# Kernel optimization log

Measured on AMD Instinct MI355X. Metric: run time of the kernel, lower is better.

## Reference

```python
import jax, jax.numpy as jnp
import numpy as np

N = 50000
E = 600000
D = 128


def gcn_conv(x, row, col, w, W, b):
    """PyG GCNConv: add self-loops (weight 1), symmetric deg^-1/2 normalization,
    linear transform, edge-weighted scatter-add aggregation, then bias."""
    n = x.shape[0]
    loop = jnp.arange(n)
    r = jnp.concatenate([row, loop])            # source nodes, [E+N]
    c = jnp.concatenate([col, loop])            # target nodes, [E+N]
    ww = jnp.concatenate([w, jnp.ones((n,), x.dtype)])
    deg = jax.ops.segment_sum(ww, c, num_segments=n)          # weighted in-degree
    dinv = jnp.where(deg > 0, jax.lax.rsqrt(deg), jnp.zeros_like(deg))
    norm = dinv[r] * ww * dinv[c]               # [E+N]
    xl = x @ W                                  # [n, D_out]
    msg = norm[:, None] * xl[r]                 # gather + scale, [E+N, D_out]
    out = jax.ops.segment_sum(msg, c, num_segments=n)
    return out + b


def setup_inputs() -> dict:
    key = jax.random.key(0)
    ks = jax.random.split(key, 12)
    x = jax.random.normal(ks[0], (N, D), dtype=jnp.float32)
    edge_index = jax.random.randint(ks[1], (2, E), 0, N, dtype=jnp.int64)
    edge_weights = jax.random.uniform(ks[2], (E,), dtype=jnp.float32)
    s = 1.0 / np.sqrt(D)
    W1 = jax.random.uniform(ks[3], (D, D), jnp.float32, -s, s)
    b1 = jnp.zeros((D,), jnp.float32)
    W2 = jax.random.uniform(ks[4], (D, D), jnp.float32, -s, s)
    b2 = jnp.zeros((D,), jnp.float32)
    W3 = jax.random.uniform(ks[5], (D, D), jnp.float32, -s, s)
    b3 = jnp.zeros((D,), jnp.float32)
    prelu_w = jnp.array(0.25, jnp.float32)
    return {"x": x, "edge_index": edge_index, "edge_weights": edge_weights,
            "W1": W1, "b1": b1, "W2": W2, "b2": b2, "W3": W3, "b3": b3,
            "prelu_w": prelu_w}


def reference(x, edge_index, edge_weights, W1, b1, W2, b2, W3, b3, prelu_w):
    row, col = edge_index[0], edge_index[1]
    # layer 1: GCNConv -> (dropout: eval, identity) -> ELU
    h = gcn_conv(x, row, col, edge_weights, W1, b1)
    h = jax.nn.elu(h)
    # layer 2: GCNConv -> GELU (torch default = exact erf)
    h = gcn_conv(h, row, col, edge_weights, W2, b2)
    h = jax.nn.gelu(h, approximate=False)
    # layer 3: GCNConv -> PReLU (learnable scalar slope)
    h = gcn_conv(h, row, col, edge_weights, W3, b3)
    h = jnp.where(h >= 0, h, prelu_w * h)
    return h
```

## Files before the change

### kernel.cpp

```cpp
#include <hip/hip_runtime.h>
#include <hip/hip_fp16.h>
#include <math.h>

constexpr int D = 128;

struct __align__(16) H8 { __half2 h[4]; };
struct __align__(8)  H4 { __half2 a, b; };


__device__ __forceinline__ int detect64(const int* __restrict__ ei) {
  int z = 0;
#pragma unroll
  for (int i = 0; i < 8; ++i) z |= ei[2 * i + 1];
  return (z == 0) ? 1 : 0;
}

__device__ __forceinline__ void load_edge(const int* __restrict__ ei, int e, int nE,
                                          int m64, int n, int& r, int& c) {
  if (m64) { r = ei[2 * (size_t)e]; c = ei[2 * ((size_t)nE + e)]; }
  else     { r = ei[(size_t)e];     c = ei[(size_t)nE + e]; }
  r = min(max(r, 0), n - 1);
  c = min(max(c, 0), n - 1);
}

__global__ void k_zero(int* __restrict__ cnt, int n) {
  int i = blockIdx.x * blockDim.x + threadIdx.x;
  if (i < n) cnt[i] = 0;
}

__global__ void k_pos(const int* __restrict__ ei, int* __restrict__ cnt,
                      int2* __restrict__ rc, int* __restrict__ pos, int nE, int n) {
  int e = blockIdx.x * blockDim.x + threadIdx.x;
  if (e >= nE) return;
  int m64 = detect64(ei);
  int r, c;
  load_edge(ei, e, nE, m64, n, r, c);
  rc[e] = make_int2(r, c);
  pos[e] = atomicAdd(&cnt[c], 1);
}

__global__ void k_scan1(const int* __restrict__ cnt, int* __restrict__ offs,
                        int* __restrict__ bsum, int n) {
  __shared__ int s[256];
  int t = threadIdx.x;
  int i = blockIdx.x * 256 + t;
  int v = (i < n) ? cnt[i] : 0;
  s[t] = v;
  __syncthreads();
  for (int off = 1; off < 256; off <<= 1) {
    int x = 0;
    if (t >= off) x = s[t - off];
    __syncthreads();
    if (t >= off) s[t] += x;
    __syncthreads();
  }
  if (i < n) offs[i] = s[t] - v;
  if (t == 255) bsum[blockIdx.x] = s[255];
}

__global__ void k_scan2(const int* __restrict__ bsum, int* __restrict__ boff, int nb) {
  __shared__ int s[256];
  int t = threadIdx.x;
  int v = (t < nb) ? bsum[t] : 0;
  s[t] = v;
  __syncthreads();
  for (int off = 1; off < 256; off <<= 1) {
    int x = 0;
    if (t >= off) x = s[t - off];
    __syncthreads();
    if (t >= off) s[t] += x;
    __syncthreads();
  }
  if (t < nb) boff[t] = s[t] - v;
}

__global__ void k_scan3(int* __restrict__ offs, const int* __restrict__ boff, int n, int nE) {
  int i = blockIdx.x * 256 + threadIdx.x;
  if (i < n) offs[i] += boff[blockIdx.x];
  if (i == 0) offs[n] = nE;
}

__global__ void k_fill(const int2* __restrict__ rc, const int* __restrict__ pos,
                       const float* __restrict__ w, const int* __restrict__ offs,
                       int2* __restrict__ ecf, int nE) {
  int e = blockIdx.x * blockDim.x + threadIdx.x;
  if (e >= nE) return;
  int2 p = rc[e];
  int idx = offs[p.y] + pos[e];
  ecf[idx] = make_int2(p.x, __float_as_int(w[e]));
}

__global__ void k_degdinv(const int2* __restrict__ ecf, const int* __restrict__ offs,
                          float* __restrict__ dinv, int n) {
  int i = blockIdx.x * blockDim.x + threadIdx.x;
  if (i >= n) return;
  float s = 1.0f;
  int e1 = offs[i + 1];
  for (int e = offs[i]; e < e1; ++e) s += __int_as_float(ecf[e].y);
  dinv[i] = rsqrtf(s);
}

template <int ACT>
__device__ __forceinline__ float act_f(float x) {
  if (ACT == 1) return x > 0.f ? x : expm1f(x);
  if (ACT == 2) return 0.5f * x * (1.0f + erff(x * 0.70710678118654752440f));
  return x;
}

template <int ACT>
__global__ __launch_bounds__(256, 2) void k_gemm(const float* __restrict__ A,
                                                 const float* __restrict__ W,
                                                 __half* __restrict__ Y, int n) {
  __shared__ float As[128 * 33];
  __shared__ float Ws[32 * 128];
  const int tid = threadIdx.x;
  const int row0 = blockIdx.x * 128;
  const int tc = tid & 15;
  const int tr = tid >> 4;

  float acc[8][8];
#pragma unroll
  for (int i = 0; i < 8; ++i)
#pragma unroll
    for (int j = 0; j < 8; ++j) acc[i][j] = 0.f;

  for (int kt = 0; kt < 4; ++kt) {
#pragma unroll
    for (int i = 0; i < 4; ++i) {
      int idx = tid + i * 256;
      int r = idx >> 3;
      int c4 = idx & 7;
      float4 v = make_float4(0.f, 0.f, 0.f, 0.f);
      int gr = row0 + r;
      if (gr < n) v = *(const float4*)(A + (size_t)gr * D + kt * 32 + c4 * 4);
      v.x = act_f<ACT>(v.x); v.y = act_f<ACT>(v.y);
      v.z = act_f<ACT>(v.z); v.w = act_f<ACT>(v.w);
      As[r * 33 + c4 * 4 + 0] = v.x;
      As[r * 33 + c4 * 4 + 1] = v.y;
      As[r * 33 + c4 * 4 + 2] = v.z;
      As[r * 33 + c4 * 4 + 3] = v.w;
    }
#pragma unroll
    for (int i = 0; i < 4; ++i) {
      int idx = tid + i * 256;
      int r = idx >> 5;
      int c4 = idx & 31;
      *(float4*)(&Ws[r * 128 + c4 * 4]) =
          *(const float4*)(W + (size_t)(kt * 32 + r) * D + c4 * 4);
    }
    __syncthreads();
#pragma unroll
    for (int k = 0; k < 32; ++k) {
      float a[8];
#pragma unroll
      for (int i = 0; i < 8; ++i) a[i] = As[(tr * 8 + i) * 33 + k];
      const float4 b0 = *(const float4*)(&Ws[k * 128 + tc * 4]);
      const float4 b1 = *(const float4*)(&Ws[k * 128 + tc * 4 + 64]);
#pragma unroll
      for (int i = 0; i < 8; ++i) {
        acc[i][0] += a[i] * b0.x; acc[i][1] += a[i] * b0.y;
        acc[i][2] += a[i] * b0.z; acc[i][3] += a[i] * b0.w;
        acc[i][4] += a[i] * b1.x; acc[i][5] += a[i] * b1.y;
        acc[i][6] += a[i] * b1.z; acc[i][7] += a[i] * b1.w;
      }
    }
    __syncthreads();
  }
#pragma unroll
  for (int i = 0; i < 8; ++i) {
    int gr = row0 + tr * 8 + i;
    if (gr < n) {
      H4 lo, hi;
      lo.a = __floats2half2_rn(acc[i][0], acc[i][1]);
      lo.b = __floats2half2_rn(acc[i][2], acc[i][3]);
      hi.a = __floats2half2_rn(acc[i][4], acc[i][5]);
      hi.b = __floats2half2_rn(acc[i][6], acc[i][7]);
      *(H4*)(Y + (size_t)gr * D + tc * 4) = lo;
      *(H4*)(Y + (size_t)gr * D + tc * 4 + 64) = hi;
    }
  }
}

__device__ __forceinline__ void fmacc8(float* acc, float c, const H8& y) {
  float2 f;
  f = __half22float2(y.h[0]); acc[0] += c * f.x; acc[1] += c * f.y;
  f = __half22float2(y.h[1]); acc[2] += c * f.x; acc[3] += c * f.y;
  f = __half22float2(y.h[2]); acc[4] += c * f.x; acc[5] += c * f.y;
  f = __half22float2(y.h[3]); acc[6] += c * f.x; acc[7] += c * f.y;
}

template <int PRELU>
__global__ __launch_bounds__(256) void k_agg(const __half* __restrict__ Y,
                                             const int* __restrict__ offs,
                                             const int2* __restrict__ ecf,
                                             const float* __restrict__ dinv,
                                             const float* __restrict__ bias,
                                             const float* __restrict__ pw,
                                             float* __restrict__ OUT, int n) {
  int gi = blockIdx.x * blockDim.x + threadIdx.x;
  int node = gi >> 4;
  int j = gi & 15;
  if (node >= n) return;
  float dc = dinv[node];
  float acc[8] = {0.f, 0.f, 0.f, 0.f, 0.f, 0.f, 0.f, 0.f};
  {
    H8 ys = *(const H8*)(Y + (size_t)node * D + j * 8);
    fmacc8(acc, dc, ys);
  }
  int e0 = offs[node], e1 = offs[node + 1];
  int e = e0;
  for (; e + 4 <= e1; e += 4) {
    int2 p0 = ecf[e], p1 = ecf[e + 1], p2 = ecf[e + 2], p3 = ecf[e + 3];
    float c0 = dinv[p0.x] * __int_as_float(p0.y);
    float c1 = dinv[p1.x] * __int_as_float(p1.y);
    float c2 = dinv[p2.x] * __int_as_float(p2.y);
    float c3 = dinv[p3.x] * __int_as_float(p3.y);
    H8 y0 = *(const H8*)(Y + (size_t)p0.x * D + j * 8);
    H8 y1 = *(const H8*)(Y + (size_t)p1.x * D + j * 8);
    H8 y2 = *(const H8*)(Y + (size_t)p2.x * D + j * 8);
    H8 y3 = *(const H8*)(Y + (size_t)p3.x * D + j * 8);
    fmacc8(acc, c0, y0);
    fmacc8(acc, c1, y1);
    fmacc8(acc, c2, y2);
    fmacc8(acc, c3, y3);
  }
  for (; e < e1; ++e) {
    int2 p = ecf[e];
    float c = dinv[p.x] * __int_as_float(p.y);
    H8 y = *(const H8*)(Y + (size_t)p.x * D + j * 8);
    fmacc8(acc, c, y);
  }
  float4 b0 = *(const float4*)(bias + j * 8);
  float4 b1 = *(const float4*)(bias + j * 8 + 4);
  float o[8];
  o[0] = dc * acc[0] + b0.x; o[1] = dc * acc[1] + b0.y;
  o[2] = dc * acc[2] + b0.z; o[3] = dc * acc[3] + b0.w;
  o[4] = dc * acc[4] + b1.x; o[5] = dc * acc[5] + b1.y;
  o[6] = dc * acc[6] + b1.z; o[7] = dc * acc[7] + b1.w;
  if (PRELU) {
    float wv = *pw;
#pragma unroll
    for (int i = 0; i < 8; ++i) o[i] = o[i] >= 0.f ? o[i] : wv * o[i];
  }
  *(float4*)(OUT + (size_t)node * D + j * 8)     = make_float4(o[0], o[1], o[2], o[3]);
  *(float4*)(OUT + (size_t)node * D + j * 8 + 4) = make_float4(o[4], o[5], o[6], o[7]);
}

extern "C" void kernel_launch(void* const* d_in, const int* in_sizes, int n_in,
                              void* d_out, int out_size, void* d_ws, size_t ws_size,
                              hipStream_t stream) {
  const float* x  = (const float*)d_in[0];
  const int*   ei = (const int*)d_in[1];
  const float* w  = (const float*)d_in[2];
  const float* W1 = (const float*)d_in[3];
  const float* b1 = (const float*)d_in[4];
  const float* W2 = (const float*)d_in[5];
  const float* b2 = (const float*)d_in[6];
  const float* W3 = (const float*)d_in[7];
  const float* b3 = (const float*)d_in[8];
  const float* pw = (const float*)d_in[9];
  const int N = in_sizes[0] / D;
  const int E = in_sizes[2];
  float* out = (float*)d_out;

  char* wsb = (char*)d_ws;
  size_t off = 0;
  auto alloc = [&](size_t bytes) {
    void* p = wsb + off;
    off = (off + bytes + 255) & ~(size_t)255;
    return p;
  };
  float*  dinv = (float*)alloc((size_t)N * 4);
  int*    cnt  = (int*)alloc((size_t)N * 4);
  int*    offs = (int*)alloc((size_t)(N + 1) * 4);
  int*    bsum = (int*)alloc(256 * 4);
  int*    boff = (int*)alloc(256 * 4);
  int2*   ecf  = (int2*)alloc((size_t)E * 8);
  __half* Y    = (__half*)alloc((size_t)N * D * 2);
  int2*   rc   = (int2*)Y;
  int*    pos  = (int*)((char*)Y + (size_t)E * 8);

  const int nb = (N + 255) / 256;
  const int eb = (E + 255) / 256;

  hipLaunchKernelGGL(k_zero,    dim3(nb), dim3(256), 0, stream, cnt, N);
  hipLaunchKernelGGL(k_pos,     dim3(eb), dim3(256), 0, stream, ei, cnt, rc, pos, E, N);
  hipLaunchKernelGGL(k_scan1,   dim3(nb), dim3(256), 0, stream, cnt, offs, bsum, N);
  hipLaunchKernelGGL(k_scan2,   dim3(1),  dim3(256), 0, stream, bsum, boff, nb);
  hipLaunchKernelGGL(k_scan3,   dim3(nb), dim3(256), 0, stream, offs, boff, N, E);
  hipLaunchKernelGGL(k_fill,    dim3(eb), dim3(256), 0, stream, rc, pos, w, offs, ecf, E);
  hipLaunchKernelGGL(k_degdinv, dim3(nb), dim3(256), 0, stream, ecf, offs, dinv, N);

  const int gb = (N + 127) / 128;
  const int ab = (N * 16 + 255) / 256;

  hipLaunchKernelGGL((k_gemm<0>), dim3(gb), dim3(256), 0, stream, x, W1, Y, N);
  hipLaunchKernelGGL((k_agg<0>),  dim3(ab), dim3(256), 0, stream, Y, offs, ecf, dinv, b1, pw, out, N);
  hipLaunchKernelGGL((k_gemm<1>), dim3(gb), dim3(256), 0, stream, out, W2, Y, N);
  hipLaunchKernelGGL((k_agg<0>),  dim3(ab), dim3(256), 0, stream, Y, offs, ecf, dinv, b2, pw, out, N);
  hipLaunchKernelGGL((k_gemm<2>), dim3(gb), dim3(256), 0, stream, out, W3, Y, N);
  hipLaunchKernelGGL((k_agg<1>),  dim3(ab), dim3(256), 0, stream, Y, offs, ecf, dinv, b3, pw, out, N);
}
```

Baseline: 324.4 us.

## Store intermediate layer outputs in fp16 and split each node's edges across two half-warps

Hidden activations between layers are now stored as fp16 in a separate buffer, and the GEMM reads them as fp16 and converts to fp32 before the activation. This halves the bytes written by aggregation and read by the next GEMM. Aggregation now gives each node 32 threads: two 16-lane groups take alternating edges and combine their results with a cross-lane shuffle, which doubles memory-level parallelism on the gathers. Each thread then writes four outputs instead of eight. The cost is extra fp16 rounding error in the intermediate activations, plus a shuffle reduction and twice as many threads.

```diff
diff --git a/kernel.cpp b/kernel.cpp
--- a/kernel.cpp
+++ b/kernel.cpp
@@ -107,8 +107,8 @@
   return x;
 }
 
-template <int ACT>
-__global__ __launch_bounds__(256, 2) void k_gemm(const float* __restrict__ A,
+template <int ACT, typename AT>
+__global__ __launch_bounds__(256, 2) void k_gemm(const AT* __restrict__ A,
                                                  const float* __restrict__ W,
                                                  __half* __restrict__ Y, int n) {
   __shared__ float As[128 * 33];
@@ -125,20 +125,40 @@
     for (int j = 0; j < 8; ++j) acc[i][j] = 0.f;
 
   for (int kt = 0; kt < 4; ++kt) {
-#pragma unroll
-    for (int i = 0; i < 4; ++i) {
-      int idx = tid + i * 256;
-      int r = idx >> 3;
-      int c4 = idx & 7;
-      float4 v = make_float4(0.f, 0.f, 0.f, 0.f);
-      int gr = row0 + r;
-      if (gr < n) v = *(const float4*)(A + (size_t)gr * D + kt * 32 + c4 * 4);
-      v.x = act_f<ACT>(v.x); v.y = act_f<ACT>(v.y);
-      v.z = act_f<ACT>(v.z); v.w = act_f<ACT>(v.w);
-      As[r * 33 + c4 * 4 + 0] = v.x;
-      As[r * 33 + c4 * 4 + 1] = v.y;
-      As[r * 33 + c4 * 4 + 2] = v.z;
-      As[r * 33 + c4 * 4 + 3] = v.w;
+    if constexpr (sizeof(AT) == 4) {
+#pragma unroll
+      for (int i = 0; i < 4; ++i) {
+        int idx = tid + i * 256;
+        int r = idx >> 3;
+        int c4 = idx & 7;
+        float4 v = make_float4(0.f, 0.f, 0.f, 0.f);
+        int gr = row0 + r;
+        if (gr < n) v = *(const float4*)((const float*)A + (size_t)gr * D + kt * 32 + c4 * 4);
+        As[r * 33 + c4 * 4 + 0] = act_f<ACT>(v.x);
+        As[r * 33 + c4 * 4 + 1] = act_f<ACT>(v.y);
+        As[r * 33 + c4 * 4 + 2] = act_f<ACT>(v.z);
+        As[r * 33 + c4 * 4 + 3] = act_f<ACT>(v.w);
+      }
+    } else {
+#pragma unroll
+      for (int i = 0; i < 2; ++i) {
+        int idx = tid + i * 256;
+        int r = idx >> 2;
+        int c8 = idx & 3;
+        float f[8] = {0.f, 0.f, 0.f, 0.f, 0.f, 0.f, 0.f, 0.f};
+        int gr = row0 + r;
+        if (gr < n) {
+          H8 v = *(const H8*)((const __half*)A + (size_t)gr * D + kt * 32 + c8 * 8);
+#pragma unroll
+          for (int t = 0; t < 4; ++t) {
+            float2 p = __half22float2(v.h[t]);
+            f[2 * t] = p.x; f[2 * t + 1] = p.y;
+          }
+        }
+#pragma unroll
+        for (int t = 0; t < 8; ++t)
+          As[r * 33 + c8 * 8 + t] = act_f<ACT>(f[t]);
+      }
     }
 #pragma unroll
     for (int i = 0; i < 4; ++i) {
@@ -189,28 +209,29 @@
   f = __half22float2(y.h[3]); acc[6] += c * f.x; acc[7] += c * f.y;
 }
 
-template <int PRELU>
+template <int PRELU, typename OutT>
 __global__ __launch_bounds__(256) void k_agg(const __half* __restrict__ Y,
                                              const int* __restrict__ offs,
                                              const int2* __restrict__ ecf,
                                              const float* __restrict__ dinv,
                                              const float* __restrict__ bias,
                                              const float* __restrict__ pw,
-                                             float* __restrict__ OUT, int n) {
+                                             OutT* __restrict__ OUT, int n) {
   int gi = blockIdx.x * blockDim.x + threadIdx.x;
-  int node = gi >> 4;
+  int node = gi >> 5;
+  int sub = (gi >> 4) & 1;
   int j = gi & 15;
   if (node >= n) return;
   float dc = dinv[node];
   float acc[8] = {0.f, 0.f, 0.f, 0.f, 0.f, 0.f, 0.f, 0.f};
-  {
+  if (sub == 0) {
     H8 ys = *(const H8*)(Y + (size_t)node * D + j * 8);
     fmacc8(acc, dc, ys);
   }
   int e0 = offs[node], e1 = offs[node + 1];
-  int e = e0;
-  for (; e + 4 <= e1; e += 4) {
-    int2 p0 = ecf[e], p1 = ecf[e + 1], p2 = ecf[e + 2], p3 = ecf[e + 3];
+  int e = e0 + sub;
+  for (; e + 6 < e1; e += 8) {
+    int2 p0 = ecf[e], p1 = ecf[e + 2], p2 = ecf[e + 4], p3 = ecf[e + 6];
     float c0 = dinv[p0.x] * __int_as_float(p0.y);
     float c1 = dinv[p1.x] * __int_as_float(p1.y);
     float c2 = dinv[p2.x] * __int_as_float(p2.y);
@@ -224,26 +245,34 @@
     fmacc8(acc, c2, y2);
     fmacc8(acc, c3, y3);
   }
-  for (; e < e1; ++e) {
+  for (; e < e1; e += 2) {
     int2 p = ecf[e];
     float c = dinv[p.x] * __int_as_float(p.y);
     H8 y = *(const H8*)(Y + (size_t)p.x * D + j * 8);
     fmacc8(acc, c, y);
   }
-  float4 b0 = *(const float4*)(bias + j * 8);
-  float4 b1 = *(const float4*)(bias + j * 8 + 4);
-  float o[8];
-  o[0] = dc * acc[0] + b0.x; o[1] = dc * acc[1] + b0.y;
-  o[2] = dc * acc[2] + b0.z; o[3] = dc * acc[3] + b0.w;
-  o[4] = dc * acc[4] + b1.x; o[5] = dc * acc[5] + b1.y;
-  o[6] = dc * acc[6] + b1.z; o[7] = dc * acc[7] + b1.w;
+#pragma unroll
+  for (int i = 0; i < 8; ++i) acc[i] += __shfl_xor(acc[i], 16, 64);
+  float4 b4 = *(const float4*)(bias + j * 8 + sub * 4);
+  float o[4];
+  o[0] = dc * acc[sub * 4 + 0] + b4.x;
+  o[1] = dc * acc[sub * 4 + 1] + b4.y;
+  o[2] = dc * acc[sub * 4 + 2] + b4.z;
+  o[3] = dc * acc[sub * 4 + 3] + b4.w;
   if (PRELU) {
     float wv = *pw;
 #pragma unroll
-    for (int i = 0; i < 8; ++i) o[i] = o[i] >= 0.f ? o[i] : wv * o[i];
-  }
-  *(float4*)(OUT + (size_t)node * D + j * 8)     = make_float4(o[0], o[1], o[2], o[3]);
-  *(float4*)(OUT + (size_t)node * D + j * 8 + 4) = make_float4(o[4], o[5], o[6], o[7]);
+    for (int i = 0; i < 4; ++i) o[i] = o[i] >= 0.f ? o[i] : wv * o[i];
+  }
+  if constexpr (sizeof(OutT) == 4) {
+    *(float4*)((float*)OUT + (size_t)node * D + j * 8 + sub * 4) =
+        make_float4(o[0], o[1], o[2], o[3]);
+  } else {
+    H4 hv;
+    hv.a = __floats2half2_rn(o[0], o[1]);
+    hv.b = __floats2half2_rn(o[2], o[3]);
+    *(H4*)((__half*)OUT + (size_t)node * D + j * 8 + sub * 4) = hv;
+  }
 }
 
 extern "C" void kernel_launch(void* const* d_in, const int* in_sizes, int n_in,
@@ -277,6 +306,7 @@
   int*    boff = (int*)alloc(256 * 4);
   int2*   ecf  = (int2*)alloc((size_t)E * 8);
   __half* Y    = (__half*)alloc((size_t)N * D * 2);
+  __half* h    = (__half*)alloc((size_t)N * D * 2);
   int2*   rc   = (int2*)Y;
   int*    pos  = (int*)((char*)Y + (size_t)E * 8);
 
@@ -292,12 +322,12 @@
   hipLaunchKernelGGL(k_degdinv, dim3(nb), dim3(256), 0, stream, ecf, offs, dinv, N);
 
   const int gb = (N + 127) / 128;
-  const int ab = (N * 16 + 255) / 256;
-
-  hipLaunchKernelGGL((k_gemm<0>), dim3(gb), dim3(256), 0, stream, x, W1, Y, N);
-  hipLaunchKernelGGL((k_agg<0>),  dim3(ab), dim3(256), 0, stream, Y, offs, ecf, dinv, b1, pw, out, N);
-  hipLaunchKernelGGL((k_gemm<1>), dim3(gb), dim3(256), 0, stream, out, W2, Y, N);
-  hipLaunchKernelGGL((k_agg<0>),  dim3(ab), dim3(256), 0, stream, Y, offs, ecf, dinv, b2, pw, out, N);
-  hipLaunchKernelGGL((k_gemm<2>), dim3(gb), dim3(256), 0, stream, out, W3, Y, N);
-  hipLaunchKernelGGL((k_agg<1>),  dim3(ab), dim3(256), 0, stream, Y, offs, ecf, dinv, b3, pw, out, N);
-}
+  const int ab = (N * 32 + 255) / 256;
+
+  hipLaunchKernelGGL((k_gemm<0, float>),  dim3(gb), dim3(256), 0, stream, x, W1, Y, N);
+  hipLaunchKernelGGL((k_agg<0, __half>),  dim3(ab), dim3(256), 0, stream, Y, offs, ecf, dinv, b1, pw, h, N);
+  hipLaunchKernelGGL((k_gemm<1, __half>), dim3(gb), dim3(256), 0, stream, h, W2, Y, N);
+  hipLaunchKernelGGL((k_agg<0, __half>),  dim3(ab), dim3(256), 0, stream, Y, offs, ecf, dinv, b2, pw, h, N);
+  hipLaunchKernelGGL((k_gemm<2, __half>), dim3(gb), dim3(256), 0, stream, h, W3, Y, N);
+  hipLaunchKernelGGL((k_agg<1, float>),   dim3(ab), dim3(256), 0, stream, Y, offs, ecf, dinv, b3, pw, out, N);
+}
```

Result: no change. 323.5 us (-0.3%).
